# Optimization experiments

Hardware: AMD Instinct MI355X
Metric: run time of the kernel (lower is better)

The kernel has to match this reference:

```python
import jax, jax.numpy as jnp
import numpy as np

D_MODEL = 1024
HEAD_DIM = 128
NUM_HEADS = 8


def setup_inputs() -> dict:
    key = jax.random.key(0)
    ks = jax.random.split(key, 7)
    s = 0.02
    x = jax.random.normal(ks[0], (1, 4096, D_MODEL), dtype=jnp.float32)
    Wq = jax.random.normal(ks[1], (D_MODEL, NUM_HEADS * HEAD_DIM), dtype=jnp.float32) * s
    bq = jnp.zeros((NUM_HEADS * HEAD_DIM,), dtype=jnp.float32)
    Wk = jax.random.normal(ks[2], (D_MODEL, HEAD_DIM), dtype=jnp.float32) * s
    bk = jnp.zeros((HEAD_DIM,), dtype=jnp.float32)
    Wv = jax.random.normal(ks[3], (D_MODEL, HEAD_DIM), dtype=jnp.float32) * s
    bv = jnp.zeros((HEAD_DIM,), dtype=jnp.float32)
    return {"x": x, "Wq": Wq, "bq": bq, "Wk": Wk, "bk": bk, "Wv": Wv, "bv": bv}


def reference(x, Wq, bq, Wk, bk, Wv, bv):
    b, s, _ = x.shape
    q = (x @ Wq + bq).reshape(b, s, NUM_HEADS, HEAD_DIM)  # [b,s,h,d]
    k = x @ Wk + bk  # [b,s,d] shared across heads
    v = x @ Wv + bv  # [b,s,d]
    scale = 1.0 / jnp.sqrt(jnp.float32(HEAD_DIM))
    # scores: [b,h,q,k]
    scores = jnp.einsum('bqhd,bkd->bhqk', q, k) * scale
    attn = jax.nn.softmax(scores, axis=-1)
    out = jnp.einsum('bhqk,bkd->bqhd', attn, v)  # [b,s,h,d]
    return out.reshape(b, s, NUM_HEADS * HEAD_DIM)
```

## Files before the change

### kernel.cpp

```cpp
#include <hip/hip_runtime.h>
#include <hip/hip_bf16.h>
#include <stdint.h>

#define D_MODEL 1024
#define HEAD_DIM 128
#define NUM_HEADS 8
#define SEQ 4096

using bf16x8 = __attribute__((ext_vector_type(8))) short;
using f32x4  = __attribute__((ext_vector_type(4))) float;

__device__ __forceinline__ unsigned short f32_to_bf16(float f) {
    union { float f; uint32_t u; } c{f};
    uint32_t u = c.u;
    return (unsigned short)((u + 0x7fffu + ((u >> 16) & 1u)) >> 16);
}
__device__ __forceinline__ uint32_t pack_bf16x2(float lo, float hi) {
    return (uint32_t)f32_to_bf16(lo) | ((uint32_t)f32_to_bf16(hi) << 16);
}
__device__ __forceinline__ uint32_t cvt2_bf16(float a, float b) {
#if __has_builtin(__builtin_amdgcn_cvt_pk_bf16_f32)
    auto r = __builtin_amdgcn_cvt_pk_bf16_f32(a, b);
    union { decltype(r) v; uint32_t u; } c; c.v = r;
    return c.u;
#else
    return pack_bf16x2(a, b);
#endif
}

__device__ __forceinline__ void dma16(const void* g, void* l) {
    __builtin_amdgcn_global_load_lds(
        (const __attribute__((address_space(1))) unsigned int*)g,
        (__attribute__((address_space(3))) unsigned int*)l, 16, 0, 0);
}

__global__ __launch_bounds__(256) void prep(
    const float4* __restrict__ x, int4* __restrict__ xb,
    const float* __restrict__ Wq, const float* __restrict__ Wk,
    const float* __restrict__ Wv, unsigned short* __restrict__ Wt)
{
    __shared__ unsigned short tile[64][72];
    const int t = threadIdx.x;
    if (blockIdx.x < 2048) {
        int i = blockIdx.x * 256 + t;
        float4 a = x[2 * i], b = x[2 * i + 1];
        int4 o;
        o.x = (int)cvt2_bf16(a.x, a.y);
        o.y = (int)cvt2_bf16(a.z, a.w);
        o.z = (int)cvt2_bf16(b.x, b.y);
        o.w = (int)cvt2_bf16(b.z, b.w);
        xb[i] = o;
        return;
    }
    int bt = blockIdx.x - 2048;
    int ktile = bt & 15, ntile = bt >> 4;
    int k0 = ktile * 64, n0 = ntile * 64;
    const float* W; int ldw, nc0;
    if (n0 < 1024)      { W = Wq; ldw = 1024; nc0 = n0; }
    else if (n0 < 1152) { W = Wk; ldw = 128;  nc0 = n0 - 1024; }
    else                { W = Wv; ldw = 128;  nc0 = n0 - 1152; }
    int c = t & 63, r0 = t >> 6;
#pragma unroll
    for (int p = 0; p < 16; ++p) {
        int r = r0 + p * 4;
        tile[c][r] = f32_to_bf16(W[(k0 + r) * ldw + nc0 + c]);
    }
    __syncthreads();
#pragma unroll
    for (int p = 0; p < 16; ++p) {
        int rn = r0 + p * 4;
        Wt[(n0 + rn) * 1024 + k0 + c] = tile[rn][c];
    }
}

__global__ __launch_bounds__(256, 3) void qkv_gemm(
    const unsigned short* __restrict__ xb,
    const unsigned short* __restrict__ Wt,
    const float* __restrict__ bq, const float* __restrict__ bk, const float* __restrict__ bv,
    unsigned short* __restrict__ q_bf,
    unsigned short* __restrict__ k_bf,
    unsigned short* __restrict__ vt_bf)
{
    __shared__ unsigned short As[2][128 * 64];
    __shared__ unsigned short Bs[2][64 * 64];
    const int t = threadIdx.x;
    const int lane = t & 63, wave = t >> 6;
    const int l15 = lane & 15, quad = lane >> 4;
    const int m0 = blockIdx.x * 128, n0 = blockIdx.y * 64;
    const int srow_l = lane >> 3;
    const int sc_phys = lane & 7;

    f32x4 acc[2][4];
#pragma unroll
    for (int i = 0; i < 2; ++i)
#pragma unroll
        for (int j = 0; j < 4; ++j) acc[i][j] = (f32x4)0.0f;

    auto issue = [&](int k0c, int buf) {
        int c = sc_phys ^ srow_l;
#pragma unroll
        for (int p = 0; p < 4; ++p) {
            int rb = (wave * 4 + p) * 8;
            dma16(&xb[(m0 + rb + srow_l) * 1024 + k0c + c * 8], &As[buf][rb * 64]);
        }
#pragma unroll
        for (int p = 0; p < 2; ++p) {
            int rb = (wave * 2 + p) * 8;
            dma16(&Wt[(n0 + rb + srow_l) * 1024 + k0c + c * 8], &Bs[buf][rb * 64]);
        }
    };

    issue(0, 0);
    for (int kst = 0; kst < 16; ++kst) {
        const int buf = kst & 1;
        __syncthreads();
        if (kst < 15) issue((kst + 1) * 64, buf ^ 1);
#pragma unroll
        for (int ks = 0; ks < 2; ++ks) {
            bf16x8 a[2], b[4];
#pragma unroll
            for (int mt = 0; mt < 2; ++mt)
                a[mt] = *(const bf16x8*)&As[buf][(wave * 32 + mt * 16 + l15) * 64 + (((ks * 4 + quad) ^ (l15 & 7)) * 8)];
#pragma unroll
            for (int nt = 0; nt < 4; ++nt)
                b[nt] = *(const bf16x8*)&Bs[buf][(nt * 16 + l15) * 64 + (((ks * 4 + quad) ^ (l15 & 7)) * 8)];
#pragma unroll
            for (int mt = 0; mt < 2; ++mt)
#pragma unroll
                for (int nt = 0; nt < 4; ++nt)
                    acc[mt][nt] = __builtin_amdgcn_mfma_f32_16x16x32_bf16(a[mt], b[nt], acc[mt][nt], 0, 0, 0);
        }
    }

    const float qscale = 0.08838834764831843f * 1.4426950408889634f;
    if (blockIdx.y < 16) {
#pragma unroll
        for (int mt = 0; mt < 2; ++mt)
#pragma unroll
            for (int nt = 0; nt < 4; ++nt) {
                int row = m0 + wave * 32 + mt * 16 + quad * 4;
                int col = n0 + nt * 16 + l15;
                float b = bq[col];
                uint32_t u01 = cvt2_bf16((acc[mt][nt][0] + b) * qscale, (acc[mt][nt][1] + b) * qscale);
                uint32_t u23 = cvt2_bf16((acc[mt][nt][2] + b) * qscale, (acc[mt][nt][3] + b) * qscale);
                q_bf[(row + 0) * 1024 + col] = (unsigned short)u01;
                q_bf[(row + 1) * 1024 + col] = (unsigned short)(u01 >> 16);
                q_bf[(row + 2) * 1024 + col] = (unsigned short)u23;
                q_bf[(row + 3) * 1024 + col] = (unsigned short)(u23 >> 16);
            }
    } else if (blockIdx.y < 18) {
#pragma unroll
        for (int mt = 0; mt < 2; ++mt)
#pragma unroll
            for (int nt = 0; nt < 4; ++nt) {
                int row = m0 + wave * 32 + mt * 16 + quad * 4;
                int col = n0 + nt * 16 + l15 - 1024;
                float b = bk[col];
                uint32_t u01 = cvt2_bf16(acc[mt][nt][0] + b, acc[mt][nt][1] + b);
                uint32_t u23 = cvt2_bf16(acc[mt][nt][2] + b, acc[mt][nt][3] + b);
                k_bf[(row + 0) * 128 + col] = (unsigned short)u01;
                k_bf[(row + 1) * 128 + col] = (unsigned short)(u01 >> 16);
                k_bf[(row + 2) * 128 + col] = (unsigned short)u23;
                k_bf[(row + 3) * 128 + col] = (unsigned short)(u23 >> 16);
            }
    } else {
        unsigned short* T = (unsigned short*)As;
        __syncthreads();
#pragma unroll
        for (int mt = 0; mt < 2; ++mt)
#pragma unroll
            for (int nt = 0; nt < 4; ++nt) {
                int lrow = wave * 32 + mt * 16 + quad * 4;
                int lc = nt * 16 + l15;
                float b = bv[n0 + lc - 1152];
                uint32_t u01 = cvt2_bf16(acc[mt][nt][0] + b, acc[mt][nt][1] + b);
                uint32_t u23 = cvt2_bf16(acc[mt][nt][2] + b, acc[mt][nt][3] + b);
                T[lc * 136 + lrow + 0] = (unsigned short)u01;
                T[lc * 136 + lrow + 1] = (unsigned short)(u01 >> 16);
                T[lc * 136 + lrow + 2] = (unsigned short)u23;
                T[lc * 136 + lrow + 3] = (unsigned short)(u23 >> 16);
            }
        __syncthreads();
        int vx = blockIdx.y - 18;
#pragma unroll
        for (int p = 0; p < 4; ++p) {
            int lc = p * 16 + (t >> 4);
            int r0 = (t & 15) * 8;
            int4 d = *(const int4*)&T[lc * 136 + r0];
            *(int4*)&vt_bf[(vx * 64 + lc) * 4096 + m0 + r0] = d;
        }
    }
}

__global__ __launch_bounds__(512, 2) void mqa_attn(
    const unsigned short* __restrict__ q_bf,
    const unsigned short* __restrict__ k_bf,
    const unsigned short* __restrict__ vt_bf,
    float* __restrict__ out)
{
    __shared__ unsigned short Ks[2][2][64 * 128];
    __shared__ unsigned short Vs[2][144 * 64];
    __shared__ unsigned short Ps[8][2][16 * 72];
    const int t = threadIdx.x;
    const int lane = t & 63, wave = t >> 6;
    const int l15 = lane & 15, quad = lane >> 4;
    const int half = wave >> 2, w2 = wave & 3;
    const int qbase = blockIdx.x * 32 + (w2 & 1) * 16;
    const int h0 = blockIdx.y * 4 + (w2 >> 1) * 2;
    const int kbase = half * 2048;

    const int krow_l = lane >> 4;
    const int kc_phys = lane & 15;
    const int vrow_l = lane >> 3;
    const int vc_phys = lane & 7;

    for (int i = t; i < 2048; i += 512) {
        int hh = i >> 10, rr = (i >> 6) & 15, cc = i & 63;
        Vs[hh][(128 + rr) * 64 + cc] = (rr == 0) ? (unsigned short)0x3F80 : (unsigned short)0;
    }

    bf16x8 qf[2][4];
    {
        int qrow = qbase + l15;
#pragma unroll
        for (int g = 0; g < 2; ++g)
#pragma unroll
            for (int ks = 0; ks < 4; ++ks)
                qf[g][ks] = *(const bf16x8*)&q_bf[qrow * 1024 + (h0 + g) * 128 + ks * 32 + quad * 8];
    }

    f32x4 o[2][9];
#pragma unroll
    for (int g = 0; g < 2; ++g)
#pragma unroll
        for (int d = 0; d < 9; ++d) o[g][d] = (f32x4)0.0f;

    auto issueK = [&](int kt, int buf) {
#pragma unroll
        for (int p = 0; p < 4; ++p) {
            int row = w2 * 16 + p * 4 + krow_l;
            int c = kc_phys ^ (row & 15);
            dma16(&k_bf[(kt + row) * 128 + c * 8], &Ks[half][buf][(w2 * 16 + p * 4) * 128]);
        }
    };
    auto issueV = [&](int kt) {
#pragma unroll
        for (int p = 0; p < 4; ++p) {
            int row = w2 * 32 + p * 8 + vrow_l;
            int c = vc_phys ^ vrow_l;
            dma16(&vt_bf[row * 4096 + kt + c * 8], &Vs[half][(w2 * 32 + p * 8) * 64]);
        }
    };

    issueK(kbase, 0);
    for (int it = 0; it < 32; ++it) {
        const int buf = it & 1;
        __syncthreads();
        issueV(kbase + it * 64);
        const bool pk = (it + 1 < 32);
        if (pk) issueK(kbase + (it + 1) * 64, buf ^ 1);

        f32x4 s[2][4];
#pragma unroll
        for (int g = 0; g < 2; ++g)
#pragma unroll
            for (int nt = 0; nt < 4; ++nt) s[g][nt] = (f32x4)0.0f;
#pragma unroll
        for (int ks = 0; ks < 4; ++ks)
#pragma unroll
            for (int nt = 0; nt < 4; ++nt) {
                int row = nt * 16 + l15;
                bf16x8 kb = *(const bf16x8*)&Ks[half][buf][row * 128 + (((ks * 4 + quad) ^ l15) * 8)];
                s[0][nt] = __builtin_amdgcn_mfma_f32_16x16x32_bf16(qf[0][ks], kb, s[0][nt], 0, 0, 0);
                s[1][nt] = __builtin_amdgcn_mfma_f32_16x16x32_bf16(qf[1][ks], kb, s[1][nt], 0, 0, 0);
            }

#pragma unroll
        for (int g = 0; g < 2; ++g) {
            unsigned short* P = &Ps[wave][g][0];
#pragma unroll
            for (int nt = 0; nt < 4; ++nt) {
                float p0 = __builtin_amdgcn_exp2f(s[g][nt][0]);
                float p1 = __builtin_amdgcn_exp2f(s[g][nt][1]);
                float p2 = __builtin_amdgcn_exp2f(s[g][nt][2]);
                float p3 = __builtin_amdgcn_exp2f(s[g][nt][3]);
                uint32_t u01 = cvt2_bf16(p0, p1);
                uint32_t u23 = cvt2_bf16(p2, p3);
                int col = nt * 16 + l15;
                P[(quad * 4 + 0) * 72 + col] = (unsigned short)u01;
                P[(quad * 4 + 1) * 72 + col] = (unsigned short)(u01 >> 16);
                P[(quad * 4 + 2) * 72 + col] = (unsigned short)u23;
                P[(quad * 4 + 3) * 72 + col] = (unsigned short)(u23 >> 16);
            }
        }
        asm volatile("s_waitcnt lgkmcnt(0)" ::: "memory");
        if (pk) asm volatile("s_waitcnt vmcnt(4)" ::: "memory");
        else    asm volatile("s_waitcnt vmcnt(0)" ::: "memory");

#pragma unroll
        for (int ks = 0; ks < 2; ++ks) {
            bf16x8 pa0 = *(const bf16x8*)&Ps[wave][0][l15 * 72 + ks * 32 + quad * 8];
            bf16x8 pa1 = *(const bf16x8*)&Ps[wave][1][l15 * 72 + ks * 32 + quad * 8];
#pragma unroll
            for (int d = 0; d < 9; ++d) {
                int row = d * 16 + l15;
                bf16x8 vb = *(const bf16x8*)&Vs[half][row * 64 + (((ks * 4 + quad) ^ (l15 & 7)) * 8)];
                o[0][d] = __builtin_amdgcn_mfma_f32_16x16x32_bf16(pa0, vb, o[0][d], 0, 0, 0);
                o[1][d] = __builtin_amdgcn_mfma_f32_16x16x32_bf16(pa1, vb, o[1][d], 0, 0, 0);
            }
        }
    }

    __syncthreads();
    float* Xo = (float*)&Ks[0][0][0];
    float* Xl = (float*)&Vs[0][0];
    if (half == 1) {
#pragma unroll
        for (int g = 0; g < 2; ++g) {
#pragma unroll
            for (int d = 0; d < 8; ++d)
                *(f32x4*)&Xo[((w2 * 16 + g * 8 + d) * 64 + lane) * 4] = o[g][d];
            *(f32x4*)&Xl[((w2 * 2 + g) * 64 + lane) * 4] = o[g][8];
        }
    }
    __syncthreads();
    if (half == 0) {
#pragma unroll
        for (int g = 0; g < 2; ++g) {
#pragma unroll
            for (int d = 0; d < 8; ++d)
                o[g][d] += *(const f32x4*)&Xo[((w2 * 16 + g * 8 + d) * 64 + lane) * 4];
            f32x4 o8 = o[g][8] + *(const f32x4*)&Xl[((w2 * 2 + g) * 64 + lane) * 4];
#pragma unroll
            for (int r = 0; r < 4; ++r) {
                float l = __shfl(o8[r], lane & 48, 64);
                float inv = 1.0f / l;
                int row = qbase + quad * 4 + r;
#pragma unroll
                for (int d = 0; d < 8; ++d)
                    out[row * 1024 + (h0 + g) * 128 + d * 16 + l15] = o[g][d][r] * inv;
            }
        }
    }
}

extern "C" void kernel_launch(void* const* d_in, const int* in_sizes, int n_in,
                              void* d_out, int out_size, void* d_ws, size_t ws_size,
                              hipStream_t stream) {
    const float* x  = (const float*)d_in[0];
    const float* Wq = (const float*)d_in[1];
    const float* bq = (const float*)d_in[2];
    const float* Wk = (const float*)d_in[3];
    const float* bk = (const float*)d_in[4];
    const float* Wv = (const float*)d_in[5];
    const float* bv = (const float*)d_in[6];
    float* out = (float*)d_out;

    char* ws = (char*)d_ws;
    unsigned short* xb = (unsigned short*)(ws);
    unsigned short* Wt = (unsigned short*)(ws + 8388608);
    unsigned short* qb = (unsigned short*)(ws + 11010048);
    unsigned short* kb = (unsigned short*)(ws + 19398656);
    unsigned short* vt = (unsigned short*)(ws + 20447232);

    prep<<<2368, 256, 0, stream>>>((const float4*)x, (int4*)xb, Wq, Wk, Wv, Wt);
    qkv_gemm<<<dim3(32, 20), 256, 0, stream>>>(xb, Wt, bq, bk, bv, qb, kb, vt);
    mqa_attn<<<dim3(SEQ / 32, 2), 512, 0, stream>>>(qb, kb, vt, out);
}
```

Before: 185.9 us.

## Enlarge QKV GEMM tiles, register ones vector for row sums, transpose score MFMA

The QKV projection GEMM moves from 128x64 to 128x128 block tiles with a 2x2 wave layout and 64x64 per-wave tiles. This raises operand reuse and halves the grid, at the cost of more accumulator registers and lower occupancy. In attention, the LDS-resident ones rows used for the softmax denominator become a register constant fed to an extra MFMA, which shrinks the V shared buffer. The score MFMA operands are swapped so P can be stored with packed 8-byte LDS writes instead of scalar 2-byte stores; the V-transpose store is vectorized the same way.

```diff
diff --git a/kernel.cpp b/kernel.cpp
--- a/kernel.cpp
+++ b/kernel.cpp
@@ -73,7 +73,7 @@
     }
 }
 
-__global__ __launch_bounds__(256, 3) void qkv_gemm(
+__global__ __launch_bounds__(256, 2) void qkv_gemm(
     const unsigned short* __restrict__ xb,
     const unsigned short* __restrict__ Wt,
     const float* __restrict__ bq, const float* __restrict__ bk, const float* __restrict__ bv,
@@ -81,18 +81,20 @@
     unsigned short* __restrict__ k_bf,
     unsigned short* __restrict__ vt_bf)
 {
-    __shared__ unsigned short As[2][128 * 64];
-    __shared__ unsigned short Bs[2][64 * 64];
+    __shared__ unsigned short SM[32768];
+    unsigned short* As = SM;
+    unsigned short* Bs = SM + 16384;
     const int t = threadIdx.x;
     const int lane = t & 63, wave = t >> 6;
     const int l15 = lane & 15, quad = lane >> 4;
-    const int m0 = blockIdx.x * 128, n0 = blockIdx.y * 64;
+    const int m0 = blockIdx.x * 128, n0 = blockIdx.y * 128;
+    const int wm = (wave >> 1) * 64, wn = (wave & 1) * 64;
     const int srow_l = lane >> 3;
     const int sc_phys = lane & 7;
 
-    f32x4 acc[2][4];
-#pragma unroll
-    for (int i = 0; i < 2; ++i)
+    f32x4 acc[4][4];
+#pragma unroll
+    for (int i = 0; i < 4; ++i)
 #pragma unroll
         for (int j = 0; j < 4; ++j) acc[i][j] = (f32x4)0.0f;
 
@@ -101,12 +103,8 @@
 #pragma unroll
         for (int p = 0; p < 4; ++p) {
             int rb = (wave * 4 + p) * 8;
-            dma16(&xb[(m0 + rb + srow_l) * 1024 + k0c + c * 8], &As[buf][rb * 64]);
-        }
-#pragma unroll
-        for (int p = 0; p < 2; ++p) {
-            int rb = (wave * 2 + p) * 8;
-            dma16(&Wt[(n0 + rb + srow_l) * 1024 + k0c + c * 8], &Bs[buf][rb * 64]);
+            dma16(&xb[(m0 + rb + srow_l) * 1024 + k0c + c * 8], &As[buf * 8192 + rb * 64]);
+            dma16(&Wt[(n0 + rb + srow_l) * 1024 + k0c + c * 8], &Bs[buf * 8192 + rb * 64]);
         }
     };
 
@@ -117,15 +115,15 @@
         if (kst < 15) issue((kst + 1) * 64, buf ^ 1);
 #pragma unroll
         for (int ks = 0; ks < 2; ++ks) {
-            bf16x8 a[2], b[4];
-#pragma unroll
-            for (int mt = 0; mt < 2; ++mt)
-                a[mt] = *(const bf16x8*)&As[buf][(wave * 32 + mt * 16 + l15) * 64 + (((ks * 4 + quad) ^ (l15 & 7)) * 8)];
+            bf16x8 a[4], b[4];
+#pragma unroll
+            for (int mt = 0; mt < 4; ++mt)
+                a[mt] = *(const bf16x8*)&As[buf * 8192 + (wm + mt * 16 + l15) * 64 + (((ks * 4 + quad) ^ (l15 & 7)) * 8)];
 #pragma unroll
             for (int nt = 0; nt < 4; ++nt)
-                b[nt] = *(const bf16x8*)&Bs[buf][(nt * 16 + l15) * 64 + (((ks * 4 + quad) ^ (l15 & 7)) * 8)];
-#pragma unroll
-            for (int mt = 0; mt < 2; ++mt)
+                b[nt] = *(const bf16x8*)&Bs[buf * 8192 + (wn + nt * 16 + l15) * 64 + (((ks * 4 + quad) ^ (l15 & 7)) * 8)];
+#pragma unroll
+            for (int mt = 0; mt < 4; ++mt)
 #pragma unroll
                 for (int nt = 0; nt < 4; ++nt)
                     acc[mt][nt] = __builtin_amdgcn_mfma_f32_16x16x32_bf16(a[mt], b[nt], acc[mt][nt], 0, 0, 0);
@@ -133,13 +131,13 @@
     }
 
     const float qscale = 0.08838834764831843f * 1.4426950408889634f;
-    if (blockIdx.y < 16) {
-#pragma unroll
-        for (int mt = 0; mt < 2; ++mt)
-#pragma unroll
-            for (int nt = 0; nt < 4; ++nt) {
-                int row = m0 + wave * 32 + mt * 16 + quad * 4;
-                int col = n0 + nt * 16 + l15;
+    if (blockIdx.y < 8) {
+#pragma unroll
+        for (int mt = 0; mt < 4; ++mt)
+#pragma unroll
+            for (int nt = 0; nt < 4; ++nt) {
+                int row = m0 + wm + mt * 16 + quad * 4;
+                int col = n0 + wn + nt * 16 + l15;
                 float b = bq[col];
                 uint32_t u01 = cvt2_bf16((acc[mt][nt][0] + b) * qscale, (acc[mt][nt][1] + b) * qscale);
                 uint32_t u23 = cvt2_bf16((acc[mt][nt][2] + b) * qscale, (acc[mt][nt][3] + b) * qscale);
@@ -148,13 +146,13 @@
                 q_bf[(row + 2) * 1024 + col] = (unsigned short)u23;
                 q_bf[(row + 3) * 1024 + col] = (unsigned short)(u23 >> 16);
             }
-    } else if (blockIdx.y < 18) {
-#pragma unroll
-        for (int mt = 0; mt < 2; ++mt)
-#pragma unroll
-            for (int nt = 0; nt < 4; ++nt) {
-                int row = m0 + wave * 32 + mt * 16 + quad * 4;
-                int col = n0 + nt * 16 + l15 - 1024;
+    } else if (blockIdx.y == 8) {
+#pragma unroll
+        for (int mt = 0; mt < 4; ++mt)
+#pragma unroll
+            for (int nt = 0; nt < 4; ++nt) {
+                int row = m0 + wm + mt * 16 + quad * 4;
+                int col = wn + nt * 16 + l15;
                 float b = bk[col];
                 uint32_t u01 = cvt2_bf16(acc[mt][nt][0] + b, acc[mt][nt][1] + b);
                 uint32_t u23 = cvt2_bf16(acc[mt][nt][2] + b, acc[mt][nt][3] + b);
@@ -164,42 +162,39 @@
                 k_bf[(row + 3) * 128 + col] = (unsigned short)(u23 >> 16);
             }
     } else {
-        unsigned short* T = (unsigned short*)As;
+        unsigned short* T = SM;
         __syncthreads();
 #pragma unroll
-        for (int mt = 0; mt < 2; ++mt)
-#pragma unroll
-            for (int nt = 0; nt < 4; ++nt) {
-                int lrow = wave * 32 + mt * 16 + quad * 4;
-                int lc = nt * 16 + l15;
-                float b = bv[n0 + lc - 1152];
-                uint32_t u01 = cvt2_bf16(acc[mt][nt][0] + b, acc[mt][nt][1] + b);
-                uint32_t u23 = cvt2_bf16(acc[mt][nt][2] + b, acc[mt][nt][3] + b);
-                T[lc * 136 + lrow + 0] = (unsigned short)u01;
-                T[lc * 136 + lrow + 1] = (unsigned short)(u01 >> 16);
-                T[lc * 136 + lrow + 2] = (unsigned short)u23;
-                T[lc * 136 + lrow + 3] = (unsigned short)(u23 >> 16);
+        for (int mt = 0; mt < 4; ++mt)
+#pragma unroll
+            for (int nt = 0; nt < 4; ++nt) {
+                int lrow = wm + mt * 16 + quad * 4;
+                int lc = wn + nt * 16 + l15;
+                float b = bv[lc];
+                uint2 u;
+                u.x = cvt2_bf16(acc[mt][nt][0] + b, acc[mt][nt][1] + b);
+                u.y = cvt2_bf16(acc[mt][nt][2] + b, acc[mt][nt][3] + b);
+                *(uint2*)&T[lc * 136 + lrow] = u;
             }
         __syncthreads();
-        int vx = blockIdx.y - 18;
-#pragma unroll
-        for (int p = 0; p < 4; ++p) {
-            int lc = p * 16 + (t >> 4);
-            int r0 = (t & 15) * 8;
-            int4 d = *(const int4*)&T[lc * 136 + r0];
-            *(int4*)&vt_bf[(vx * 64 + lc) * 4096 + m0 + r0] = d;
-        }
-    }
-}
-
-__global__ __launch_bounds__(512, 2) void mqa_attn(
+        int dr = t >> 1;
+#pragma unroll
+        for (int p = 0; p < 8; ++p) {
+            int idx = (t & 1) * 8 + p;
+            int4 d = *(const int4*)&T[dr * 136 + idx * 8];
+            *(int4*)&vt_bf[dr * 4096 + m0 + idx * 8] = d;
+        }
+    }
+}
+
+__global__ __launch_bounds__(512, 1) void mqa_attn(
     const unsigned short* __restrict__ q_bf,
     const unsigned short* __restrict__ k_bf,
     const unsigned short* __restrict__ vt_bf,
     float* __restrict__ out)
 {
     __shared__ unsigned short Ks[2][2][64 * 128];
-    __shared__ unsigned short Vs[2][144 * 64];
+    __shared__ unsigned short Vs[2][128 * 64];
     __shared__ unsigned short Ps[8][2][16 * 72];
     const int t = threadIdx.x;
     const int lane = t & 63, wave = t >> 6;
@@ -214,10 +209,9 @@
     const int vrow_l = lane >> 3;
     const int vc_phys = lane & 7;
 
-    for (int i = t; i < 2048; i += 512) {
-        int hh = i >> 10, rr = (i >> 6) & 15, cc = i & 63;
-        Vs[hh][(128 + rr) * 64 + cc] = (rr == 0) ? (unsigned short)0x3F80 : (unsigned short)0;
-    }
+    bf16x8 onesf;
+#pragma unroll
+    for (int j = 0; j < 8; ++j) onesf[j] = (l15 == 0) ? (short)0x3F80 : (short)0;
 
     bf16x8 qf[2][4];
     {
@@ -271,8 +265,8 @@
             for (int nt = 0; nt < 4; ++nt) {
                 int row = nt * 16 + l15;
                 bf16x8 kb = *(const bf16x8*)&Ks[half][buf][row * 128 + (((ks * 4 + quad) ^ l15) * 8)];
-                s[0][nt] = __builtin_amdgcn_mfma_f32_16x16x32_bf16(qf[0][ks], kb, s[0][nt], 0, 0, 0);
-                s[1][nt] = __builtin_amdgcn_mfma_f32_16x16x32_bf16(qf[1][ks], kb, s[1][nt], 0, 0, 0);
+                s[0][nt] = __builtin_amdgcn_mfma_f32_16x16x32_bf16(kb, qf[0][ks], s[0][nt], 0, 0, 0);
+                s[1][nt] = __builtin_amdgcn_mfma_f32_16x16x32_bf16(kb, qf[1][ks], s[1][nt], 0, 0, 0);
             }
 
 #pragma unroll
@@ -284,13 +278,10 @@
                 float p1 = __builtin_amdgcn_exp2f(s[g][nt][1]);
                 float p2 = __builtin_amdgcn_exp2f(s[g][nt][2]);
                 float p3 = __builtin_amdgcn_exp2f(s[g][nt][3]);
-                uint32_t u01 = cvt2_bf16(p0, p1);
-                uint32_t u23 = cvt2_bf16(p2, p3);
-                int col = nt * 16 + l15;
-                P[(quad * 4 + 0) * 72 + col] = (unsigned short)u01;
-                P[(quad * 4 + 1) * 72 + col] = (unsigned short)(u01 >> 16);
-                P[(quad * 4 + 2) * 72 + col] = (unsigned short)u23;
-                P[(quad * 4 + 3) * 72 + col] = (unsigned short)(u23 >> 16);
+                uint2 u;
+                u.x = cvt2_bf16(p0, p1);
+                u.y = cvt2_bf16(p2, p3);
+                *(uint2*)&P[l15 * 72 + nt * 16 + quad * 4] = u;
             }
         }
         asm volatile("s_waitcnt lgkmcnt(0)" ::: "memory");
@@ -302,12 +293,14 @@
             bf16x8 pa0 = *(const bf16x8*)&Ps[wave][0][l15 * 72 + ks * 32 + quad * 8];
             bf16x8 pa1 = *(const bf16x8*)&Ps[wave][1][l15 * 72 + ks * 32 + quad * 8];
 #pragma unroll
-            for (int d = 0; d < 9; ++d) {
+            for (int d = 0; d < 8; ++d) {
                 int row = d * 16 + l15;
                 bf16x8 vb = *(const bf16x8*)&Vs[half][row * 64 + (((ks * 4 + quad) ^ (l15 & 7)) * 8)];
                 o[0][d] = __builtin_amdgcn_mfma_f32_16x16x32_bf16(pa0, vb, o[0][d], 0, 0, 0);
                 o[1][d] = __builtin_amdgcn_mfma_f32_16x16x32_bf16(pa1, vb, o[1][d], 0, 0, 0);
             }
+            o[0][8] = __builtin_amdgcn_mfma_f32_16x16x32_bf16(pa0, onesf, o[0][8], 0, 0, 0);
+            o[1][8] = __builtin_amdgcn_mfma_f32_16x16x32_bf16(pa1, onesf, o[1][8], 0, 0, 0);
         }
     }
 
@@ -364,6 +357,6 @@
     unsigned short* vt = (unsigned short*)(ws + 20447232);
 
     prep<<<2368, 256, 0, stream>>>((const float4*)x, (int4*)xb, Wq, Wk, Wv, Wt);
-    qkv_gemm<<<dim3(32, 20), 256, 0, stream>>>(xb, Wt, bq, bk, bv, qb, kb, vt);
+    qkv_gemm<<<dim3(32, 10), 256, 0, stream>>>(xb, Wt, bq, bk, bv, qb, kb, vt);
     mqa_attn<<<dim3(SEQ / 32, 2), 512, 0, stream>>>(qb, kb, vt, out);
 }
```

After: 183.0 us (median of 2 runs). No clear change (-1.6%).
